# Kernel optimization log

Measured on AMD Instinct MI355X. Metric: run time of the kernel, lower is better.

## Reference

```python
import jax, jax.numpy as jnp
import numpy as np

B, T, I, H = 128, 1024, 128, 512


def setup_inputs():
    key = jax.random.key(0)
    ks = jax.random.split(key, 7)
    x = jax.random.normal(ks[0], (B, T, I), jnp.float32)
    mask = (jax.random.uniform(ks[1], (B, T)) < 0.1).astype(jnp.int32)
    # lengths sorted DESCENDING (required by the per-step batch truncation); max == T
    length = jnp.sort(jax.random.randint(ks[2], (B,), T // 2, T + 1))[::-1]
    length = length.at[0].set(T)
    s = 1.0 / np.sqrt(H)
    W_ih = jax.random.uniform(ks[3], (4 * H, I), jnp.float32, -s, s)
    W_hh = jax.random.uniform(ks[4], (4 * H, H), jnp.float32, -s, s)
    b_ih = jax.random.uniform(ks[5], (4 * H,), jnp.float32, -s, s)
    b_hh = jax.random.uniform(ks[6], (4 * H,), jnp.float32, -s, s)
    return dict(input=x, mask=mask, length=length, W_ih=W_ih, W_hh=W_hh, b_ih=b_ih, b_hh=b_hh)


def _boundary_mask(mask, length):
    # mask[:,0]=0 then scatter 1 at end index (length-1), as in the torch code
    Bq = mask.shape[0]
    m = mask.astype(jnp.float32)
    m = m.at[:, 0].set(0.0)
    m = m.at[jnp.arange(Bq), length - 1].set(1.0)
    return m


def _gather_index(m):
    # Replicates the pad-to-max-words while-loop + nonzero/gather pipeline.
    # The loop extends a suffix of ones until each row has exactly max_w ones;
    # equivalently: set to 1 every position whose suffix zero-count <= (max_w - num).
    Bq, Tq = m.shape
    word_nums = m.sum(axis=1)
    max_w = word_nums.max()
    need = max_w - word_nums
    zcum = jnp.cumsum((1.0 - m)[:, ::-1], axis=1)[:, ::-1]  # zeros in suffix (inclusive)
    padded = jnp.where(zcum <= need[:, None], 1.0, m)
    K = int(max_w)  # every row now has exactly K ones
    # column indices of the ones, in ascending order (row-major nonzero order)
    cols = jnp.argsort(1.0 - padded, axis=1, stable=True)[:, :K]
    # index = row*T + col - 1, gathered from the flattened embeddings (torch wraps -1)
    flat_idx = (jnp.arange(Bq)[:, None] * Tq + cols - 1) % (Bq * Tq)
    return flat_idx, word_nums, K


def _run_lstm(x, m, active, W_ih, W_hh, b_ih, b_hh):
    # Masked per-timestep LSTMCell: h,c are zeroed at boundaries (mask==0) before
    # each step; rows with t >= length are frozen (emulates batch_size_t truncation
    # for descending-sorted lengths) and their embeddings stay zero.
    Bq = x.shape[0]
    Hq = W_hh.shape[1]
    h0 = jnp.zeros((Bq, Hq), x.dtype)

    def step(carry, xs):
        h, c = carry
        x_t, m_t, a_t = xs
        h = h * m_t[:, None]
        c = c * m_t[:, None]
        gates = x_t @ W_ih.T + h @ W_hh.T + b_ih + b_hh
        i, f, g, o = jnp.split(gates, 4, axis=1)  # torch gate order i,f,g,o
        c2 = jax.nn.sigmoid(f) * c + jax.nn.sigmoid(i) * jnp.tanh(g)
        h2 = jax.nn.sigmoid(o) * jnp.tanh(c2)
        a = a_t[:, None]
        return (a * h2 + (1.0 - a) * h, a * c2 + (1.0 - a) * c), a * h2

    _, emb = jax.lax.scan(step, (h0, h0), (x.transpose(1, 0, 2), m.T, active.T))
    return emb.transpose(1, 0, 2)  # [B, T, H]


def reference(input, mask, length, W_ih, W_hh, b_ih, b_hh):
    Bq, Tq, _ = input.shape
    Hq = W_hh.shape[1]
    m = _boundary_mask(mask, length)
    active = (jnp.arange(Tq)[None, :] < length[:, None]).astype(input.dtype)
    emb = _run_lstm(input, m, active, W_ih, W_hh, b_ih, b_hh)
    flat_idx, word_nums, K = _gather_index(m)
    out = emb.reshape(Bq * Tq, Hq)[flat_idx]  # [B, K, H]
    return out, word_nums
```

## Files before the change

### kernel.cpp

```cpp
#include <hip/hip_runtime.h>
#include <math.h>

#define BB 128
#define TT 1024
#define II 128
#define HH 512
#define GG 2048
#define BT (BB*TT)
#define LMAX 10
#define NBUCK 20

#define BM 128
#define BN 128
#define KCH 128

typedef unsigned short u16;
typedef __attribute__((ext_vector_type(4))) u16 u16x4;
typedef __attribute__((ext_vector_type(8))) u16 u16x8;
typedef __attribute__((ext_vector_type(8))) short bf16x8;
typedef __attribute__((ext_vector_type(4))) float f32x4;

typedef __attribute__((address_space(3))) unsigned int lds_u32;
typedef __attribute__((address_space(1))) const unsigned int gbl_u32;

__device__ __forceinline__ void gload16(const void* g, void* l) {
    __builtin_amdgcn_global_load_lds((gbl_u32*)g, (lds_u32*)l, 16, 0, 0);
}

__device__ __forceinline__ float rcpf(float x) { return __builtin_amdgcn_rcpf(x); }
__device__ __forceinline__ float sigf(float v) { return rcpf(1.0f + __expf(-v)); }
__device__ __forceinline__ float tanhfast(float x) {
    float e = __expf(2.0f * x);
    return 1.0f - 2.0f * rcpf(e + 1.0f);
}

__device__ __forceinline__ u16 f2b(float f) {
    unsigned int x = __float_as_uint(f);
    return (u16)((x + 0x7fffu + ((x >> 16) & 1u)) >> 16);
}

__host__ __device__ __forceinline__ int buck_cap(int bkt, int CAP0) {
    if (bkt == 0) return CAP0;
    if (bkt == 1) return 2048;
    if (bkt == 2) return 256;
    if (bkt == 3) return 128;
    if (bkt <= 9) return 64;
    if (bkt == 10) return 2048;
    if (bkt == 11) return 512;
    if (bkt == 12) return 128;
    return 64;
}
__host__ __device__ __forceinline__ int buck_off(int bkt, int CAP0) {
    int o = 0;
    for (int i = 0; i < bkt; ++i) o += buck_cap(i, CAP0);
    return o;
}
#define LIST_EXTRA (2048 + 256 + 128 + 6*64 + 2048 + 512 + 128 + 7*64)

__device__ __forceinline__ int block_scan_excl(int* ws4, int tid, int v, int* total) {
    int lane = tid & 63, wv = tid >> 6;
    int incl = v;
#pragma unroll
    for (int s = 1; s < 64; s <<= 1) {
        int u = __shfl_up(incl, (unsigned)s, 64);
        if (lane >= s) incl += u;
    }
    __syncthreads();
    if (lane == 63) ws4[wv] = incl;
    __syncthreads();
    int base = 0, tot = 0;
#pragma unroll
    for (int i = 0; i < 4; ++i) { int t = ws4[i]; if (i < wv) base += t; tot += t; }
    *total = tot;
    return base + incl - v;
}

__global__ __launch_bounds__(256) void k_prep(
    const int* __restrict__ mask, const int* __restrict__ length,
    const float* __restrict__ x, float* __restrict__ wnOut,
    int* __restrict__ levelCount, int2* __restrict__ levelList,
    int* __restrict__ slotOf, u16* __restrict__ xb, float* __restrict__ out,
    const float* __restrict__ Wih, const float* __restrict__ Whh,
    u16* __restrict__ wihb, u16* __restrict__ whhb,
    int K, int R, int CAP0) {
    int tid = threadIdx.x;
    if (blockIdx.x >= BB) {
        int i = (blockIdx.x - BB) * 256 + tid;
        const int NW = GG * II / 4;
        const int NH = GG * HH / 4;
        if (i < NW) {
            float4 v = ((const float4*)Wih)[i];
            u16x4 u = { f2b(v.x), f2b(v.y), f2b(v.z), f2b(v.w) };
            ((u16x4*)wihb)[i] = u;
        } else if (i < NW + NH) {
            int j = i - NW;
            float4 v = ((const float4*)Whh)[j];
            u16x4 u = { f2b(v.x), f2b(v.y), f2b(v.z), f2b(v.w) };
            ((u16x4*)whhb)[j] = u;
        }
        return;
    }

    __shared__ unsigned char sm[TT];
    __shared__ unsigned char sne[TT];
    __shared__ u16 sgp[TT];
    __shared__ int ws4[4];
    __shared__ int cnt[NBUCK], cnt2[NBUCK], bas[NBUCK], boff[NBUCK];
    __shared__ u16 spos[256];
    __shared__ u16 zlist[256];
    __shared__ int zn;

    int b = blockIdx.x;
    int len = length[b];
    int t0 = tid * 4;
    if (tid == 0) zn = 0;
    if (tid < NBUCK) { cnt[tid] = 0; cnt2[tid] = 0; boff[tid] = buck_off(tid, CAP0); }

    int4 mk = ((const int4*)(mask + (size_t)b * TT))[tid];
    int mraw[4] = { mk.x, mk.y, mk.z, mk.w };
    unsigned char mv[4];
    int lzero = 0;
#pragma unroll
    for (int j = 0; j < 4; ++j) {
        int t = t0 + j;
        unsigned char m = (t == len - 1) ? 1 : ((t == 0) ? 0 : (mraw[j] != 0));
        mv[j] = m;
        sm[t] = m;
        sgp[t] = 0;
        lzero += !m;
    }

    int Z;
    int zbase = block_scan_excl(ws4, tid, lzero, &Z);
    int wn = TT - Z;
    if (tid == 0) wnOut[b] = (float)wn;
    int need = K - wn;

    int psel[4];
    int lpad = 0;
    {
        int zb = zbase;
#pragma unroll
        for (int j = 0; j < 4; ++j) {
            int sel = mv[j] | ((Z - zb) <= need ? 1 : 0);
            psel[j] = sel;
            lpad += sel;
            zb += !mv[j];
        }
    }
    int ptot;
    int pbase = block_scan_excl(ws4, tid, lpad, &ptot);
    {
        int k = pbase;
#pragma unroll
        for (int j = 0; j < 4; ++j) {
            int t = t0 + j;
            if (psel[j]) {
                sgp[t - 1] = (u16)(k + 1);
                if (t - 1 >= len) {
                    int zi = atomicAdd(&zn, 1);
                    if (zi < 256) zlist[zi] = (u16)k;
                }
                ++k;
            }
        }
    }
    __syncthreads();

    int nev[4], lvlv[4];
    int lne = 0;
#pragma unroll
    for (int j = 0; j < 4; ++j) {
        int t = t0 + j;
        int ne = 0;
        if (t < len) {
            int tt = t;
            ne = sgp[tt] != 0;
            while (!ne && tt + 1 < TT && tt + 1 < len && sm[tt + 1]) { ++tt; ne = sgp[tt] != 0; }
        }
        nev[j] = ne;
        sne[t] = (unsigned char)ne;
        lne += ne;
        int l = 0;
        if (mv[j]) { int tt = t; while (tt >= 0 && sm[tt] && l < LMAX - 1) { ++l; --tt; } }
        lvlv[j] = l;
    }

    int ntot;
    int nbase = block_scan_excl(ws4, tid, lne, &ntot);
    {
        int r = nbase;
        int sv[4];
#pragma unroll
        for (int j = 0; j < 4; ++j) {
            if (nev[j]) { sv[j] = b * R + r; if (r < 256) spos[r] = (u16)(t0 + j); }
            else sv[j] = -1;
            r += nev[j];
        }
        *(int4*)(slotOf + (size_t)b * TT + t0) = make_int4(sv[0], sv[1], sv[2], sv[3]);
    }
    __syncthreads();

    int bktv[4];
#pragma unroll
    for (int j = 0; j < 4; ++j) {
        bktv[j] = -1;
        if (nev[j]) {
            int t = t0 + j;
            int pred = (t + 1 < TT) && sm[t + 1] && sne[t + 1];
            int bkt = pred ? (10 + lvlv[j]) : lvlv[j];
            bktv[j] = bkt;
            atomicAdd(&cnt[bkt], 1);
        }
    }
    __syncthreads();
    if (tid < NBUCK) bas[tid] = cnt[tid] ? atomicAdd(&levelCount[tid], cnt[tid]) : 0;
    __syncthreads();
#pragma unroll
    for (int j = 0; j < 4; ++j) if (nev[j]) {
        int t = t0 + j;
        int bkt = bktv[j];
        int r = atomicAdd(&cnt2[bkt], 1);
        int idx = bas[bkt] + r;
        unsigned int y = ((bkt >= 10) ? 0x80000000u : 0u) | (unsigned int)sgp[t];
        if (idx < buck_cap(bkt, CAP0)) levelList[boff[bkt] + idx] = make_int2(b * TT + t, (int)y);
    }
    __syncthreads();

    int nv = (ntot < 256 ? ntot : 256) * 16;
    for (int idx = tid; idx < nv; idx += 256) {
        int r = idx >> 4, part = idx & 15;
        int t = spos[r];
        const float* src = x + ((size_t)b * TT + t) * II + part * 8;
        float4 v0 = ((const float4*)src)[0];
        float4 v1 = ((const float4*)src)[1];
        u16x8 u = { f2b(v0.x), f2b(v0.y), f2b(v0.z), f2b(v0.w),
                    f2b(v1.x), f2b(v1.y), f2b(v1.z), f2b(v1.w) };
        *(u16x8*)(xb + ((size_t)b * R + r) * II + part * 8) = u;
    }
    int znv = zn < 256 ? zn : 256;
    for (int idx = tid; idx < znv * 128; idx += 256) {
        int e = idx >> 7, q = idx & 127;
        ((float4*)(out + ((size_t)b * K + zlist[e]) * HH))[q] = make_float4(0.f, 0.f, 0.f, 0.f);
    }
}

template<int HASH>
__device__ __forceinline__ void gemm_tile(
    const int2* __restrict__ list, int nrow, int jg,
    const u16* __restrict__ xb, const u16* __restrict__ wihb, const u16* __restrict__ whhb,
    const float* __restrict__ bih, const float* __restrict__ bhh,
    const int* __restrict__ slotOf, u16* __restrict__ hb, float* __restrict__ cbuf,
    float* __restrict__ out, int K,
    u16* As, u16* Bs, int* sSlot, int* sPrev, int* sAux) {
    int tid = threadIdx.x;
    if (tid < BM) {
        int2 e = list[(tid < nrow) ? tid : 0];
        int pos = e.x;
        sSlot[tid] = slotOf[pos];
        sPrev[tid] = HASH ? slotOf[pos - 1] : 0;
        unsigned int y = (unsigned int)e.y;
        int grank = (int)(y & 0xFFFFu);
        sAux[tid] = (int)((y & 0x80000000u) | (unsigned int)(grank ? ((pos >> 10) * K + grank) : 0));
    }
    __syncthreads();

    int w = tid >> 6, l = tid & 63;
    int lrow = l >> 4;
    int cbyte = (l & 15) << 4;
    f32x4 acc[2][8];
#pragma unroll
    for (int rb = 0; rb < 2; ++rb)
#pragma unroll
        for (int cb = 0; cb < 8; ++cb) acc[rb][cb] = (f32x4)0.f;

    const int nch = HASH ? 5 : 1;
    for (int kc = 0; kc < nch; ++kc) {
        bool fromX = (kc == 0);
        int koff = kc * KCH - II;
#pragma unroll
        for (int i = 0; i < 8; ++i) {
            int rr = (w << 5) + (i << 2) + lrow;
            int so = cbyte ^ ((rr & 7) << 4);
            const char* srcA = fromX
                ? (const char*)(xb + (size_t)sSlot[rr] * II) + so
                : (const char*)(hb + (size_t)sPrev[rr] * HH + koff) + so;
            gload16(srcA, (char*)As + (w << 13) + (i << 10));
            int gj = (rr >> 5) * HH + jg * 32 + (rr & 31);
            const char* srcB = fromX
                ? (const char*)(wihb + (size_t)gj * II) + so
                : (const char*)(whhb + (size_t)gj * HH + koff) + so;
            gload16(srcB, (char*)Bs + (w << 13) + (i << 10));
        }
        __syncthreads();
#pragma unroll
        for (int s = 0; s < 4; ++s) {
            bf16x8 af[2], bfr[8];
#pragma unroll
            for (int rb = 0; rb < 2; ++rb) {
                int rr = w * 32 + rb * 16 + (l & 15);
                int byte = rr * 256 + ((s * 64 + (l >> 4) * 16) ^ ((rr & 7) << 4));
                af[rb] = *(const bf16x8*)((const char*)As + byte);
            }
#pragma unroll
            for (int cb = 0; cb < 8; ++cb) {
                int rr = cb * 16 + (l & 15);
                int byte = rr * 256 + ((s * 64 + (l >> 4) * 16) ^ ((rr & 7) << 4));
                bfr[cb] = *(const bf16x8*)((const char*)Bs + byte);
            }
#pragma unroll
            for (int rb = 0; rb < 2; ++rb)
#pragma unroll
                for (int cb = 0; cb < 8; ++cb)
                    acc[rb][cb] = __builtin_amdgcn_mfma_f32_16x16x32_bf16(
                        af[rb], bfr[cb], acc[rb][cb], 0, 0, 0);
        }
        if (kc + 1 < nch) __syncthreads();
    }

    int u = l & 15;
    int h0 = jg * 32 + u;
    float b_i[2], b_f[2], b_g[2], b_o[2];
#pragma unroll
    for (int h = 0; h < 2; ++h) {
        int hc = h0 + h * 16;
        b_i[h] = bih[hc] + bhh[hc];
        b_f[h] = bih[HH + hc] + bhh[HH + hc];
        b_g[h] = bih[2 * HH + hc] + bhh[2 * HH + hc];
        b_o[h] = bih[3 * HH + hc] + bhh[3 * HH + hc];
    }
#pragma unroll
    for (int rb = 0; rb < 2; ++rb) {
#pragma unroll
        for (int r = 0; r < 4; ++r) {
            int m = w * 32 + rb * 16 + (l >> 4) * 4 + r;
            if (m < nrow) {
                int aux = sAux[m];
                int oi = aux & 0x7FFFFFFF;
                int sp = HASH ? sPrev[m] : 0;
                int sl = sSlot[m];
#pragma unroll
                for (int h = 0; h < 2; ++h) {
                    int hc = h0 + h * 16;
                    float gi = acc[rb][0 + h][r] + b_i[h];
                    float gf = acc[rb][2 + h][r] + b_f[h];
                    float gg = acc[rb][4 + h][r] + b_g[h];
                    float go = acc[rb][6 + h][r] + b_o[h];
                    float cin = HASH ? cbuf[(size_t)sp * HH + hc] : 0.f;
                    float c2 = sigf(gf) * cin + sigf(gi) * tanhfast(gg);
                    float h2 = sigf(go) * tanhfast(c2);
                    if (oi) out[(size_t)(oi - 1) * HH + hc] = h2;
                    if (aux < 0) {
                        hb[(size_t)sl * HH + hc] = f2b(h2);
                        cbuf[(size_t)sl * HH + hc] = c2;
                    }
                }
            }
        }
    }
}

template<int HASH>
__global__ __launch_bounds__(256) void k_dual(
    int bktA, int offA, int capA, int bktB, int offB, int capB,
    const int* __restrict__ levelCount, const int2* __restrict__ levelList,
    const u16* __restrict__ xb, const u16* __restrict__ wihb, const u16* __restrict__ whhb,
    const float* __restrict__ bih, const float* __restrict__ bhh,
    const int* __restrict__ slotOf, u16* __restrict__ hb, float* __restrict__ cbuf,
    float* __restrict__ out, int K) {
    __shared__ __align__(16) u16 As[BM * KCH];
    __shared__ __align__(16) u16 Bs[BN * KCH];
    __shared__ int sSlot[BM], sPrev[BM], sAux[BM];
    int ntA = (capA + BM - 1) / BM;
    int bx = blockIdx.x;
    const int2* lst;
    int n, base;
    if (bx < ntA) {
        n = levelCount[bktA]; if (n > capA) n = capA;
        base = bx * BM;
        lst = levelList + offA;
    } else {
        n = levelCount[bktB]; if (n > capB) n = capB;
        base = (bx - ntA) * BM;
        lst = levelList + offB;
    }
    if (base >= n) return;
    gemm_tile<HASH>(lst + base, min(BM, n - base), blockIdx.y,
                    xb, wihb, whhb, bih, bhh, slotOf, hb, cbuf, out, K,
                    As, Bs, sSlot, sPrev, sAux);
}

__global__ __launch_bounds__(256) void k_tail59(
    int CAP0, const int* __restrict__ levelCount, const int2* __restrict__ levelList,
    const u16* __restrict__ xb, const u16* __restrict__ wihb, const u16* __restrict__ whhb,
    const float* __restrict__ bih, const float* __restrict__ bhh,
    const int* __restrict__ slotOf, u16* __restrict__ hb, float* __restrict__ cbuf,
    float* __restrict__ out, int K, int* __restrict__ bar) {
    __shared__ __align__(16) u16 As[BM * KCH];
    __shared__ __align__(16) u16 Bs[BN * KCH];
    __shared__ int sSlot[BM], sPrev[BM], sAux[BM];
    int tid = threadIdx.x;
    int iter = 0;
    for (int l = 5; l <= 9; ++l) {
        int bkt = (blockIdx.x == 0) ? (10 + l) : l;
        int cap = buck_cap(bkt, CAP0);
        int n = levelCount[bkt]; if (n > cap) n = cap;
        if (n > 0) {
            gemm_tile<1>(levelList + buck_off(bkt, CAP0), min(BM, n), blockIdx.y,
                         xb, wihb, whhb, bih, bhh, slotOf, hb, cbuf, out, K,
                         As, Bs, sSlot, sPrev, sAux);
        }
        int rem = 0;
        for (int j = l + 1; j <= 9; ++j) {
            int a = levelCount[10 + j]; if (a > buck_cap(10 + j, CAP0)) a = buck_cap(10 + j, CAP0);
            int c = levelCount[j];      if (c > buck_cap(j, CAP0))      c = buck_cap(j, CAP0);
            rem += a + c;
        }
        ++iter;
        if (rem == 0) return;
        __threadfence();
        __syncthreads();
        if (tid == 0) {
            __hip_atomic_fetch_add(bar, 1, __ATOMIC_RELEASE, __HIP_MEMORY_SCOPE_AGENT);
            int target = 32 * iter;
            while (__hip_atomic_load(bar, __ATOMIC_ACQUIRE, __HIP_MEMORY_SCOPE_AGENT) < target) {
                __builtin_amdgcn_s_sleep(1);
            }
        }
        __syncthreads();
        __threadfence();
    }
}

extern "C" void kernel_launch(void* const* d_in, const int* in_sizes, int n_in,
                              void* d_out, int out_size, void* d_ws, size_t ws_size,
                              hipStream_t stream) {
    const float* x    = (const float*)d_in[0];
    const int* mask   = (const int*)d_in[1];
    const int* length = (const int*)d_in[2];
    const float* Wih  = (const float*)d_in[3];
    const float* Whh  = (const float*)d_in[4];
    const float* bih  = (const float*)d_in[5];
    const float* bhh  = (const float*)d_in[6];
    float* out = (float*)d_out;

    int K = (out_size - BB) / (BB * HH);
    int R = K + 64;
    int SLOTS = BB * R;
    int CAP0 = SLOTS;

    char* basep = (char*)d_ws;
    size_t off = 0;
    auto take = [&](size_t bytes) -> char* {
        off = (off + 255) & ~(size_t)255;
        char* p = basep + off;
        off += bytes;
        return p;
    };
    int* slotOf      = (int*)take((size_t)BT * 4);
    int* levelCount  = (int*)take((NBUCK + 1) * 4);
    int2* levelList  = (int2*)take((size_t)(CAP0 + LIST_EXTRA) * 8);
    u16* xb          = (u16*)take((size_t)SLOTS * II * 2);
    u16* hb          = (u16*)take((size_t)SLOTS * HH * 2);
    float* cbuf      = (float*)take((size_t)SLOTS * HH * 4);
    u16* wihb        = (u16*)take((size_t)GG * II * 2);
    u16* whhb        = (u16*)take((size_t)GG * HH * 2);
    int* bar         = levelCount + NBUCK;
    (void)ws_size; (void)in_sizes; (void)n_in;

    hipMemsetAsync(levelCount, 0, (NBUCK + 1) * 4, stream);

    const int NWCVT = (GG * (II + HH) / 4 + 255) / 256;
    k_prep<<<BB + NWCVT, 256, 0, stream>>>(
        mask, length, x, out + (size_t)BB * K * HH,
        levelCount, levelList, slotOf, xb, out, Wih, Whh, wihb, whhb, K, R, CAP0);

    {
        int oS = buck_off(10, CAP0), cS = buck_cap(10, CAP0);
        int ntS = (cS + BM - 1) / BM, ntL = (CAP0 + BM - 1) / BM;
        k_dual<0><<<dim3(ntS + ntL, GG / BN), 256, 0, stream>>>(
            10, oS, cS, 0, 0, CAP0, levelCount, levelList,
            xb, wihb, whhb, bih, bhh, slotOf, hb, cbuf, out, K);
    }
    for (int l = 1; l <= 4; ++l) {
        int oS = buck_off(10 + l, CAP0), cS = buck_cap(10 + l, CAP0);
        int oL = buck_off(l, CAP0),      cL = buck_cap(l, CAP0);
        int ntS = (cS + BM - 1) / BM, ntL = (cL + BM - 1) / BM;
        k_dual<1><<<dim3(ntS + ntL, GG / BN), 256, 0, stream>>>(
            10 + l, oS, cS, l, oL, cL, levelCount, levelList,
            xb, wihb, whhb, bih, bhh, slotOf, hb, cbuf, out, K);
    }
    k_tail59<<<dim3(2, GG / BN), 256, 0, stream>>>(
        CAP0, levelCount, levelList, xb, wihb, whhb, bih, bhh,
        slotOf, hb, cbuf, out, K, bar);
}
```

Before: 95.25 us.

## Remap dual-GEMM blocks across XCDs and fold levels 3-4 into persistent tail kernel

The dual-bucket GEMM launch now uses a 1D grid whose block index is decoded so that the 16 gate-column tiles of one row tile are spread with consistent XCD assignment (bid&7 picks the row-tile group). The aim is better L2 locality per XCD for shared hidden/x rows. Levels 3 and 4 move from separate launches into the persistent k_tail kernel, which now covers levels 3-9, and buckets 3-9 get a uniform capacity of 128. This saves two kernel launches, but levels 3-4 now run on only 2x16 blocks with grid barriers, which could be slower if those levels hold many rows.

```diff
diff --git a/kernel.cpp b/kernel.cpp
--- a/kernel.cpp
+++ b/kernel.cpp
@@ -43,8 +43,7 @@
     if (bkt == 0) return CAP0;
     if (bkt == 1) return 2048;
     if (bkt == 2) return 256;
-    if (bkt == 3) return 128;
-    if (bkt <= 9) return 64;
+    if (bkt <= 9) return 128;
     if (bkt == 10) return 2048;
     if (bkt == 11) return 512;
     if (bkt == 12) return 128;
@@ -55,7 +54,7 @@
     for (int i = 0; i < bkt; ++i) o += buck_cap(i, CAP0);
     return o;
 }
-#define LIST_EXTRA (2048 + 256 + 128 + 6*64 + 2048 + 512 + 128 + 7*64)
+#define LIST_EXTRA (2048 + 256 + 7*128 + 2048 + 512 + 128 + 7*64)
 
 __device__ __forceinline__ int block_scan_excl(int* ws4, int tid, int v, int* total) {
     int lane = tid & 63, wv = tid >> 6;
@@ -362,7 +361,8 @@
 
 template<int HASH>
 __global__ __launch_bounds__(256) void k_dual(
-    int bktA, int offA, int capA, int bktB, int offB, int capB,
+    int bktA, int offA, int capA, int ntA,
+    int bktB, int offB, int capB, int ntTot,
     const int* __restrict__ levelCount, const int2* __restrict__ levelList,
     const u16* __restrict__ xb, const u16* __restrict__ wihb, const u16* __restrict__ whhb,
     const float* __restrict__ bih, const float* __restrict__ bhh,
@@ -371,26 +371,29 @@
     __shared__ __align__(16) u16 As[BM * KCH];
     __shared__ __align__(16) u16 Bs[BN * KCH];
     __shared__ int sSlot[BM], sPrev[BM], sAux[BM];
-    int ntA = (capA + BM - 1) / BM;
-    int bx = blockIdx.x;
+    int bid = (int)blockIdx.x;
+    int xcd = bid & 7, q = bid >> 3;
+    int jg = q & 15;
+    int v = ((q >> 4) << 3) + xcd;
+    if (v >= ntTot) return;
     const int2* lst;
     int n, base;
-    if (bx < ntA) {
+    if (v < ntA) {
         n = levelCount[bktA]; if (n > capA) n = capA;
-        base = bx * BM;
+        base = v * BM;
         lst = levelList + offA;
     } else {
         n = levelCount[bktB]; if (n > capB) n = capB;
-        base = (bx - ntA) * BM;
+        base = (v - ntA) * BM;
         lst = levelList + offB;
     }
     if (base >= n) return;
-    gemm_tile<HASH>(lst + base, min(BM, n - base), blockIdx.y,
+    gemm_tile<HASH>(lst + base, min(BM, n - base), jg,
                     xb, wihb, whhb, bih, bhh, slotOf, hb, cbuf, out, K,
                     As, Bs, sSlot, sPrev, sAux);
 }
 
-__global__ __launch_bounds__(256) void k_tail59(
+__global__ __launch_bounds__(256) void k_tail39(
     int CAP0, const int* __restrict__ levelCount, const int2* __restrict__ levelList,
     const u16* __restrict__ xb, const u16* __restrict__ wihb, const u16* __restrict__ whhb,
     const float* __restrict__ bih, const float* __restrict__ bhh,
@@ -401,7 +404,7 @@
     __shared__ int sSlot[BM], sPrev[BM], sAux[BM];
     int tid = threadIdx.x;
     int iter = 0;
-    for (int l = 5; l <= 9; ++l) {
+    for (int l = 3; l <= 9; ++l) {
         int bkt = (blockIdx.x == 0) ? (10 + l) : l;
         int cap = buck_cap(bkt, CAP0);
         int n = levelCount[bkt]; if (n > cap) n = cap;
@@ -477,20 +480,24 @@
 
     {
         int oS = buck_off(10, CAP0), cS = buck_cap(10, CAP0);
-        int ntS = (cS + BM - 1) / BM, ntL = (CAP0 + BM - 1) / BM;
-        k_dual<0><<<dim3(ntS + ntL, GG / BN), 256, 0, stream>>>(
-            10, oS, cS, 0, 0, CAP0, levelCount, levelList,
+        int ntS = (cS + BM - 1) / BM;
+        int ntTot = ntS + (CAP0 + BM - 1) / BM;
+        int nv8 = (ntTot + 7) & ~7;
+        k_dual<0><<<dim3(nv8 * 16, 1), 256, 0, stream>>>(
+            10, oS, cS, ntS, 0, 0, CAP0, ntTot, levelCount, levelList,
             xb, wihb, whhb, bih, bhh, slotOf, hb, cbuf, out, K);
     }
-    for (int l = 1; l <= 4; ++l) {
+    for (int l = 1; l <= 2; ++l) {
         int oS = buck_off(10 + l, CAP0), cS = buck_cap(10 + l, CAP0);
         int oL = buck_off(l, CAP0),      cL = buck_cap(l, CAP0);
-        int ntS = (cS + BM - 1) / BM, ntL = (cL + BM - 1) / BM;
-        k_dual<1><<<dim3(ntS + ntL, GG / BN), 256, 0, stream>>>(
-            10 + l, oS, cS, l, oL, cL, levelCount, levelList,
+        int ntS = (cS + BM - 1) / BM;
+        int ntTot = ntS + (cL + BM - 1) / BM;
+        int nv8 = (ntTot + 7) & ~7;
+        k_dual<1><<<dim3(nv8 * 16, 1), 256, 0, stream>>>(
+            10 + l, oS, cS, ntS, l, oL, cL, ntTot, levelCount, levelList,
             xb, wihb, whhb, bih, bhh, slotOf, hb, cbuf, out, K);
     }
-    k_tail59<<<dim3(2, GG / BN), 256, 0, stream>>>(
+    k_tail39<<<dim3(2, 16), 256, 0, stream>>>(
         CAP0, levelCount, levelList, xb, wihb, whhb, bih, bhh,
         slotOf, hb, cbuf, out, K, bar);
 }
```

Measured after the change: 89.63 us (median of 2 runs). 5.9% less time.
